# Optimization experiments

Measured on AMD Instinct MI355X. Metric: run time of the kernel, lower is better.

Reference implementation:

```python
import jax, jax.numpy as jnp
import numpy as np

N_NODES = 100000
N_EDGES = 1600000
D_IN = 13      # per-localization feature dim
D_POS = 3
HIDDEN = 64
D_OUT = 64


def setup_inputs() -> dict:
    key = jax.random.key(0)
    ks = jax.random.split(key, 6)
    x_locs = jax.random.normal(ks[0], (N_NODES, D_IN), dtype=jnp.float32)
    pos_locs = jax.random.uniform(ks[1], (N_NODES, D_POS), dtype=jnp.float32)
    edge_index = jax.random.randint(ks[2], (2, N_EDGES), 0, N_NODES, dtype=jnp.int64)
    fan1 = D_IN + D_POS
    W1 = jax.random.normal(ks[3], (fan1, HIDDEN), dtype=jnp.float32) / np.sqrt(fan1)
    b1 = jnp.zeros((HIDDEN,), dtype=jnp.float32)
    W2 = jax.random.normal(ks[4], (HIDDEN, D_OUT), dtype=jnp.float32) / np.sqrt(HIDDEN)
    b2 = jnp.zeros((D_OUT,), dtype=jnp.float32)
    return {"x_locs": x_locs, "pos_locs": pos_locs, "W1": W1, "b1": b1,
            "W2": W2, "b2": b2, "edge_index": edge_index}


def reference(x_locs, pos_locs, W1, b1, W2, b2, edge_index):
    # PointNetConv (source_to_target): j = edge_index[0] (source), i = edge_index[1] (target)
    src = edge_index[0]
    dst = edge_index[1]
    # message input: [x_j, pos_j - pos_i]  -> [E, D_IN + D_POS]
    msg_in = jnp.concatenate([x_locs[src], pos_locs[src] - pos_locs[dst]], axis=-1)
    # local_nn: Linear -> ReLU -> Linear
    h = jax.nn.relu(msg_in @ W1 + b1)            # [E, HIDDEN]
    h = h @ W2 + b2                               # [E, D_OUT]
    # max aggregation per target node; empty segments get -inf
    agg = jax.ops.segment_max(h, dst, num_segments=N_NODES)  # [N, D_OUT]
    # final .relu() in LocEncoder; also maps empty (-inf) segments to 0 (PyG convention)
    return jax.nn.relu(agg)
```

## Files before the change

### kernel.cpp

```cpp
#include <hip/hip_runtime.h>


#define N_NODES 100000
#define N_EDGES 1600000
#define NB2  1563
#define NBLK 391
#define BATCH 4096
#define SCAP2 1280

typedef _Float16 half8 __attribute__((ext_vector_type(8)));
typedef float float4v __attribute__((ext_vector_type(4)));

__device__ inline int wave_incl_scan(int v, int lane) {
#pragma unroll
    for (int d = 1; d < 64; d <<= 1) {
        const int t = __shfl_up(v, d);
        if (lane >= d) v += t;
    }
    return v;
}

__global__ __launch_bounds__(256) void precompute_kernel(
    const float* __restrict__ x, const float* __restrict__ pos,
    const float* __restrict__ W1, const float* __restrict__ b1,
    _Float16* __restrict__ u16, _Float16* __restrict__ w16)
{
    const int lane = threadIdx.x & 63;
    float w1c[16];
#pragma unroll
    for (int k = 0; k < 16; ++k) w1c[k] = W1[k * 64 + lane];
    const float b1c = b1[lane];

    const int waveId = blockIdx.x * 4 + (threadIdx.x >> 6);
    const int step   = 512 * 4 * 2;

    for (int nd = waveId * 2; nd < N_NODES; nd += step) {
        const int nA = nd, nB = nd + 1;
        float mA = 0.f, mB = 0.f;
        if (lane < 13) {
            mA = x[nA * 13 + lane];
            mB = x[nB * 13 + lane];
        } else if (lane < 16) {
            mA = pos[nA * 3 + (lane - 13)];
            mB = pos[nB * 3 + (lane - 13)];
        }

        float aA = b1c, wA = 0.f, aB = b1c, wB = 0.f;
#pragma unroll
        for (int k = 0; k < 13; ++k) {
            aA = fmaf(__shfl(mA, k), w1c[k], aA);
            aB = fmaf(__shfl(mB, k), w1c[k], aB);
        }
#pragma unroll
        for (int k = 13; k < 16; ++k) {
            const float pA = __shfl(mA, k), pB = __shfl(mB, k);
            aA = fmaf(pA, w1c[k], aA);  wA = fmaf(pA, w1c[k], wA);
            aB = fmaf(pB, w1c[k], aB);  wB = fmaf(pB, w1c[k], wB);
        }
        u16[nA * 64 + lane] = (_Float16)aA;
        w16[nA * 64 + lane] = (_Float16)wA;
        u16[nB * 64 + lane] = (_Float16)aB;
        w16[nB * 64 + lane] = (_Float16)wB;
    }
}

__global__ __launch_bounds__(256) void partition_kernel(
    const int* __restrict__ ei,
    int* __restrict__ offsT,
    int* __restrict__ blockSorted)
{
    __shared__ int hist[NB2], eoff[NB2], offc[NB2];
    __shared__ int csumP[25];

    const int tid  = threadIdx.x;
    const int lane = tid & 63;
    const int wv   = tid >> 6;
    const int blk  = blockIdx.x;
    const int e0   = blk * BATCH;
    const int nn   = (N_EDGES - e0) < BATCH ? (N_EDGES - e0) : BATCH;

    for (int i = tid; i < NB2; i += 256) hist[i] = 0;
    __syncthreads();

#pragma unroll
    for (int rep = 0; rep < 4; ++rep) {
        const int base = rep * 1024 + tid * 4;
        if (base < nn) {
            const int4 d4 = *(const int4*)(ei + N_EDGES + e0 + base);
            atomicAdd(&hist[d4.x >> 6], 1);
            atomicAdd(&hist[d4.y >> 6], 1);
            atomicAdd(&hist[d4.z >> 6], 1);
            atomicAdd(&hist[d4.w >> 6], 1);
        }
    }
    __syncthreads();

    for (int c = wv; c < 25; c += 4) {
        const int idx = c * 64 + lane;
        const int val = (idx < NB2) ? hist[idx] : 0;
        const int inc = wave_incl_scan(val, lane);
        if (idx < NB2) eoff[idx] = inc;
        if (lane == 63) csumP[c] = inc;
    }
    __syncthreads();
    if (tid == 0) {
        int a = 0;
#pragma unroll
        for (int c = 0; c < 25; ++c) { const int t = csumP[c]; csumP[c] = a; a += t; }
    }
    __syncthreads();
    for (int c = wv; c < 25; c += 4) {
        const int idx = c * 64 + lane;
        if (idx < NB2) eoff[idx] += csumP[c] - hist[idx];
    }
    __syncthreads();

    for (int b = tid; b < NB2; b += 256) {
        offsT[b * NBLK + blk] = eoff[b];
        offc[b] = eoff[b];
    }
    if (tid == 0) offsT[NB2 * NBLK + blk] = nn;
    __syncthreads();

    int* dstp = blockSorted + blk * BATCH;
#pragma unroll
    for (int rep = 0; rep < 4; ++rep) {
        const int base = rep * 1024 + tid * 4;
        if (base < nn) {
            const int4 s4 = *(const int4*)(ei + e0 + base);
            const int4 d4 = *(const int4*)(ei + N_EDGES + e0 + base);
            int p;
            p = atomicAdd(&offc[d4.x >> 6], 1); dstp[p] = (s4.x << 6) | (d4.x & 63);
            p = atomicAdd(&offc[d4.y >> 6], 1); dstp[p] = (s4.y << 6) | (d4.y & 63);
            p = atomicAdd(&offc[d4.z >> 6], 1); dstp[p] = (s4.z << 6) | (d4.z & 63);
            p = atomicAdd(&offc[d4.w >> 6], 1); dstp[p] = (s4.w << 6) | (d4.w & 63);
        }
    }
}

__global__ __launch_bounds__(256, 4) void aggregate_kernel(
    const _Float16* __restrict__ u16,
    const _Float16* __restrict__ w16,
    const float* __restrict__ W2,
    const float* __restrict__ b2,
    const int*   __restrict__ offsT,
    const int*   __restrict__ blockSorted,
    float*       __restrict__ out)
{
    __shared__ int staged[SCAP2];
    __shared__ int sortedL[SCAP2];
    __shared__ int E[NBLK], G[NBLK];
    __shared__ int hist[64], nstart[64], hoff[64];
    __shared__ int csum[8];
    __shared__ int totT;

    const int tid  = threadIdx.x;
    const int lane = tid & 63;
    const int wv   = tid >> 6;
    const int q = lane >> 4, n = lane & 15;
    const int b = blockIdx.x;
    const int node0 = b * 64;

    half8 w2f[2][4];
#pragma unroll
    for (int s = 0; s < 2; ++s)
#pragma unroll
        for (int t = 0; t < 4; ++t)
#pragma unroll
            for (int j = 0; j < 8; ++j)
                w2f[s][t][j] = (_Float16)W2[(s * 32 + q * 8 + j) * 64 + (n + 16 * t)];
    float b2c[4];
#pragma unroll
    for (int t = 0; t < 4; ++t) b2c[t] = b2[n + 16 * t];

    if (tid < 64) hist[tid] = 0;

    for (int r = tid; r < NBLK; r += 256) {
        const int lo = offsT[b * NBLK + r];
        const int hi = offsT[(b + 1) * NBLK + r];
        staged[r] = hi - lo;
        G[r] = r * BATCH + lo;
    }
    __syncthreads();
    for (int c = wv; c < 7; c += 4) {
        const int idx = c * 64 + lane;
        const int val = (idx < NBLK) ? staged[idx] : 0;
        const int inc = wave_incl_scan(val, lane);
        if (idx < NBLK) E[idx] = inc;
        if (lane == 63) csum[c] = inc;
    }
    __syncthreads();
    if (tid == 0) {
        int a = 0;
#pragma unroll
        for (int c = 0; c < 7; ++c) { const int t = csum[c]; csum[c] = a; a += t; }
        totT = a;
    }
    __syncthreads();
    for (int c = wv; c < 7; c += 4) {
        const int idx = c * 64 + lane;
        if (idx < NBLK) E[idx] += csum[c] - staged[idx];
    }
    __syncthreads();

    int T = totT; T = T < SCAP2 ? T : SCAP2;

    for (int i = tid; i < T; i += 256) {
        int lo = 0, hi = NBLK - 1;
#pragma unroll
        for (int s = 0; s < 9; ++s) {
            const int mid = (lo + hi + 1) >> 1;
            if (E[mid] <= i) lo = mid; else hi = mid - 1;
        }
        const int w = blockSorted[G[lo] + (i - E[lo])];
        staged[i] = w;
        atomicAdd(&hist[w & 63], 1);
    }
    __syncthreads();

    if (wv == 0) {
        const int v = hist[lane];
        const int inc = wave_incl_scan(v, lane);
        nstart[lane] = inc - v;
        hoff[lane]   = inc - v;
    }
    __syncthreads();
    for (int i = tid; i < T; i += 256) {
        const int w = staged[i];
        const int p = atomicAdd(&hoff[w & 63], 1);
        sortedL[p] = w >> 6;
    }
    __syncthreads();

    const half8 zero8 = {0, 0, 0, 0, 0, 0, 0, 0};

    auto compute = [&](int node, int2 sd, int src,
                       half8 ulo, half8 uhi, half8 wl, half8 wh) {
        float vmax[4] = {0.f, 0.f, 0.f, 0.f};
        int base = 0;
        while (true) {
            const int rows = (sd.y - base) < 16 ? (sd.y - base) : 16;
            if (rows > 0) {
                const half8 alo = __builtin_elementwise_max(ulo - wl, zero8);
                const half8 ahi = __builtin_elementwise_max(uhi - wh, zero8);
                float4v c2[4];
#pragma unroll
                for (int t = 0; t < 4; ++t) {
                    c2[t] = __builtin_amdgcn_mfma_f32_16x16x32_f16(
                        alo, w2f[0][t], (float4v){0.f, 0.f, 0.f, 0.f}, 0, 0, 0);
                    c2[t] = __builtin_amdgcn_mfma_f32_16x16x32_f16(
                        ahi, w2f[1][t], c2[t], 0, 0, 0);
                }
#pragma unroll
                for (int r = 0; r < 4; ++r) {
                    const int row = q * 4 + r;
#pragma unroll
                    for (int t = 0; t < 4; ++t) {
                        const float v = c2[t][r] + b2c[t];
                        if (row < rows) vmax[t] = fmaxf(vmax[t], v);
                    }
                }
            }
            base += 16;
            if (base >= sd.y) break;
            const int r2 = (sd.y - base) < 16 ? (sd.y - base) : 16;
            src = (n < r2) ? sortedL[sd.x + base + n] : 0;
            ulo = *(const half8*)(u16 + src * 64 + q * 8);
            uhi = *(const half8*)(u16 + src * 64 + 32 + q * 8);
        }
#pragma unroll
        for (int t = 0; t < 4; ++t) {
            vmax[t] = fmaxf(vmax[t], __shfl_xor(vmax[t], 16));
            vmax[t] = fmaxf(vmax[t], __shfl_xor(vmax[t], 32));
        }
        float v = vmax[0];
        v = (q == 1) ? vmax[1] : v;
        v = (q == 2) ? vmax[2] : v;
        v = (q == 3) ? vmax[3] : v;
        if (node < N_NODES) out[node * 64 + lane] = v;
    };

    const int nlbase = wv * 16;
#pragma unroll 1
    for (int g = 0; g < 16; g += 2) {
        const int nlA = nlbase + g, nlB = nlA + 1;
        const int nA = node0 + nlA, nB = node0 + nlB;
        const int2 sdA = {nstart[nlA], hist[nlA]};
        const int2 sdB = {nstart[nlB], hist[nlB]};
        const int nAc = nA < (N_NODES - 1) ? nA : (N_NODES - 1);
        const int nBc = nB < (N_NODES - 1) ? nB : (N_NODES - 1);

        const int rA = sdA.y < 16 ? sdA.y : 16;
        const int rB = sdB.y < 16 ? sdB.y : 16;
        const int srcA = (n < rA) ? sortedL[sdA.x + n] : 0;
        const int srcB = (n < rB) ? sortedL[sdB.x + n] : 0;

        const half8 ulA = *(const half8*)(u16 + srcA * 64 + q * 8);
        const half8 uhA = *(const half8*)(u16 + srcA * 64 + 32 + q * 8);
        const half8 wlA = *(const half8*)(w16 + nAc * 64 + q * 8);
        const half8 whA = *(const half8*)(w16 + nAc * 64 + 32 + q * 8);
        const half8 ulB = *(const half8*)(u16 + srcB * 64 + q * 8);
        const half8 uhB = *(const half8*)(u16 + srcB * 64 + 32 + q * 8);
        const half8 wlB = *(const half8*)(w16 + nBc * 64 + q * 8);
        const half8 whB = *(const half8*)(w16 + nBc * 64 + 32 + q * 8);

        compute(nA, sdA, srcA, ulA, uhA, wlA, whA);
        compute(nB, sdB, srcB, ulB, uhB, wlB, whB);
    }
}

extern "C" void kernel_launch(void* const* d_in, const int* in_sizes, int n_in,
                              void* d_out, int out_size, void* d_ws, size_t ws_size,
                              hipStream_t stream) {
    const float* x   = (const float*)d_in[0];
    const float* pos = (const float*)d_in[1];
    const float* W1  = (const float*)d_in[2];
    const float* b1  = (const float*)d_in[3];
    const float* W2  = (const float*)d_in[4];
    const float* b2  = (const float*)d_in[5];
    const int*   ei  = (const int*)d_in[6];

    char* ws = (char*)d_ws;
    int* blockSorted = (int*)(ws + 0);
    int* offsT       = (int*)(ws + 6406144);
    _Float16* u16 = (_Float16*)(ws + 8852480);
    _Float16* w16 = (_Float16*)(ws + 21652480);

    precompute_kernel<<<512, 256, 0, stream>>>(x, pos, W1, b1, u16, w16);
    partition_kernel<<<NBLK, 256, 0, stream>>>(ei, offsT, blockSorted);
    aggregate_kernel<<<NB2, 256, 0, stream>>>(
        u16, w16, W2, b2, offsT, blockSorted, (float*)d_out);
}
```

Measured before the change: 193.1 us.

## Replace two-level partition with global atomic bucket scatter into fixed-capacity bins

Replaces the per-batch local sort, which wrote transposed offset tables, with a single scatter kernel. It uses global atomics on per-bucket counters to write edges straight into fixed-capacity (1280) bins per 64-node group. The aggregate kernel then reads its bin contiguously, with no prefix scans or binary search. This cuts the partition work and the indirect gathers. The cost is heavy contention on global atomics across 1563 counters, an extra memset launch, and silently dropped edges if a bin overflows its capacity (the old code also capped at 1280).

```diff
diff --git a/kernel.cpp b/kernel.cpp
--- a/kernel.cpp
+++ b/kernel.cpp
@@ -4,9 +4,7 @@
 #define N_NODES 100000
 #define N_EDGES 1600000
 #define NB2  1563
-#define NBLK 391
-#define BATCH 4096
-#define SCAP2 1280
+#define CAP  1280
 
 typedef _Float16 half8 __attribute__((ext_vector_type(8)));
 typedef float float4v __attribute__((ext_vector_type(4)));
@@ -64,78 +62,24 @@
     }
 }
 
-__global__ __launch_bounds__(256) void partition_kernel(
+__global__ __launch_bounds__(256) void scatter_kernel(
     const int* __restrict__ ei,
-    int* __restrict__ offsT,
-    int* __restrict__ blockSorted)
+    int* __restrict__ gcnt,
+    int* __restrict__ sortedG)
 {
-    __shared__ int hist[NB2], eoff[NB2], offc[NB2];
-    __shared__ int csumP[25];
-
-    const int tid  = threadIdx.x;
-    const int lane = tid & 63;
-    const int wv   = tid >> 6;
-    const int blk  = blockIdx.x;
-    const int e0   = blk * BATCH;
-    const int nn   = (N_EDGES - e0) < BATCH ? (N_EDGES - e0) : BATCH;
-
-    for (int i = tid; i < NB2; i += 256) hist[i] = 0;
-    __syncthreads();
-
-#pragma unroll
-    for (int rep = 0; rep < 4; ++rep) {
-        const int base = rep * 1024 + tid * 4;
-        if (base < nn) {
-            const int4 d4 = *(const int4*)(ei + N_EDGES + e0 + base);
-            atomicAdd(&hist[d4.x >> 6], 1);
-            atomicAdd(&hist[d4.y >> 6], 1);
-            atomicAdd(&hist[d4.z >> 6], 1);
-            atomicAdd(&hist[d4.w >> 6], 1);
-        }
-    }
-    __syncthreads();
-
-    for (int c = wv; c < 25; c += 4) {
-        const int idx = c * 64 + lane;
-        const int val = (idx < NB2) ? hist[idx] : 0;
-        const int inc = wave_incl_scan(val, lane);
-        if (idx < NB2) eoff[idx] = inc;
-        if (lane == 63) csumP[c] = inc;
-    }
-    __syncthreads();
-    if (tid == 0) {
-        int a = 0;
-#pragma unroll
-        for (int c = 0; c < 25; ++c) { const int t = csumP[c]; csumP[c] = a; a += t; }
-    }
-    __syncthreads();
-    for (int c = wv; c < 25; c += 4) {
-        const int idx = c * 64 + lane;
-        if (idx < NB2) eoff[idx] += csumP[c] - hist[idx];
-    }
-    __syncthreads();
-
-    for (int b = tid; b < NB2; b += 256) {
-        offsT[b * NBLK + blk] = eoff[b];
-        offc[b] = eoff[b];
-    }
-    if (tid == 0) offsT[NB2 * NBLK + blk] = nn;
-    __syncthreads();
-
-    int* dstp = blockSorted + blk * BATCH;
-#pragma unroll
-    for (int rep = 0; rep < 4; ++rep) {
-        const int base = rep * 1024 + tid * 4;
-        if (base < nn) {
-            const int4 s4 = *(const int4*)(ei + e0 + base);
-            const int4 d4 = *(const int4*)(ei + N_EDGES + e0 + base);
-            int p;
-            p = atomicAdd(&offc[d4.x >> 6], 1); dstp[p] = (s4.x << 6) | (d4.x & 63);
-            p = atomicAdd(&offc[d4.y >> 6], 1); dstp[p] = (s4.y << 6) | (d4.y & 63);
-            p = atomicAdd(&offc[d4.z >> 6], 1); dstp[p] = (s4.z << 6) | (d4.z & 63);
-            p = atomicAdd(&offc[d4.w >> 6], 1); dstp[p] = (s4.w << 6) | (d4.w & 63);
-        }
-    }
+    const int base = (blockIdx.x * 256 + threadIdx.x) * 4;
+    if (base >= N_EDGES) return;
+    const int4 s4 = *(const int4*)(ei + base);
+    const int4 d4 = *(const int4*)(ei + N_EDGES + base);
+    int b, p;
+    b = d4.x >> 6; p = atomicAdd(&gcnt[b], 1);
+    if (p < CAP) sortedG[b * CAP + p] = (s4.x << 6) | (d4.x & 63);
+    b = d4.y >> 6; p = atomicAdd(&gcnt[b], 1);
+    if (p < CAP) sortedG[b * CAP + p] = (s4.y << 6) | (d4.y & 63);
+    b = d4.z >> 6; p = atomicAdd(&gcnt[b], 1);
+    if (p < CAP) sortedG[b * CAP + p] = (s4.z << 6) | (d4.z & 63);
+    b = d4.w >> 6; p = atomicAdd(&gcnt[b], 1);
+    if (p < CAP) sortedG[b * CAP + p] = (s4.w << 6) | (d4.w & 63);
 }
 
 __global__ __launch_bounds__(256, 4) void aggregate_kernel(
@@ -143,16 +87,13 @@
     const _Float16* __restrict__ w16,
     const float* __restrict__ W2,
     const float* __restrict__ b2,
-    const int*   __restrict__ offsT,
-    const int*   __restrict__ blockSorted,
+    const int*   __restrict__ gcnt,
+    const int*   __restrict__ sortedG,
     float*       __restrict__ out)
 {
-    __shared__ int staged[SCAP2];
-    __shared__ int sortedL[SCAP2];
-    __shared__ int E[NBLK], G[NBLK];
+    __shared__ int staged[CAP];
+    __shared__ int sortedL[CAP];
     __shared__ int hist[64], nstart[64], hoff[64];
-    __shared__ int csum[8];
-    __shared__ int totT;
 
     const int tid  = threadIdx.x;
     const int lane = tid & 63;
@@ -174,47 +115,19 @@
     for (int t = 0; t < 4; ++t) b2c[t] = b2[n + 16 * t];
 
     if (tid < 64) hist[tid] = 0;
-
-    for (int r = tid; r < NBLK; r += 256) {
-        const int lo = offsT[b * NBLK + r];
-        const int hi = offsT[(b + 1) * NBLK + r];
-        staged[r] = hi - lo;
-        G[r] = r * BATCH + lo;
-    }
-    __syncthreads();
-    for (int c = wv; c < 7; c += 4) {
-        const int idx = c * 64 + lane;
-        const int val = (idx < NBLK) ? staged[idx] : 0;
-        const int inc = wave_incl_scan(val, lane);
-        if (idx < NBLK) E[idx] = inc;
-        if (lane == 63) csum[c] = inc;
-    }
-    __syncthreads();
-    if (tid == 0) {
-        int a = 0;
-#pragma unroll
-        for (int c = 0; c < 7; ++c) { const int t = csum[c]; csum[c] = a; a += t; }
-        totT = a;
-    }
-    __syncthreads();
-    for (int c = wv; c < 7; c += 4) {
-        const int idx = c * 64 + lane;
-        if (idx < NBLK) E[idx] += csum[c] - staged[idx];
-    }
-    __syncthreads();
-
-    int T = totT; T = T < SCAP2 ? T : SCAP2;
-
-    for (int i = tid; i < T; i += 256) {
-        int lo = 0, hi = NBLK - 1;
-#pragma unroll
-        for (int s = 0; s < 9; ++s) {
-            const int mid = (lo + hi + 1) >> 1;
-            if (E[mid] <= i) lo = mid; else hi = mid - 1;
-        }
-        const int w = blockSorted[G[lo] + (i - E[lo])];
-        staged[i] = w;
-        atomicAdd(&hist[w & 63], 1);
+    __syncthreads();
+
+    const int cnt = gcnt[b];
+    const int T = cnt < CAP ? cnt : CAP;
+
+    const int nI4 = (T + 3) >> 2;
+    for (int i4 = tid; i4 < nI4; i4 += 256) {
+        const int4 v = *(const int4*)(sortedG + b * CAP + i4 * 4);
+        const int e0 = i4 * 4;
+        if (e0 + 0 < T) { staged[e0 + 0] = v.x; atomicAdd(&hist[v.x & 63], 1); }
+        if (e0 + 1 < T) { staged[e0 + 1] = v.y; atomicAdd(&hist[v.y & 63], 1); }
+        if (e0 + 2 < T) { staged[e0 + 2] = v.z; atomicAdd(&hist[v.z & 63], 1); }
+        if (e0 + 3 < T) { staged[e0 + 3] = v.w; atomicAdd(&hist[v.w & 63], 1); }
     }
     __syncthreads();
 
@@ -321,13 +234,14 @@
     const int*   ei  = (const int*)d_in[6];
 
     char* ws = (char*)d_ws;
-    int* blockSorted = (int*)(ws + 0);
-    int* offsT       = (int*)(ws + 6406144);
-    _Float16* u16 = (_Float16*)(ws + 8852480);
-    _Float16* w16 = (_Float16*)(ws + 21652480);
-
+    int* gcnt    = (int*)(ws + 0);
+    int* sortedG = (int*)(ws + 8192);
+    _Float16* u16 = (_Float16*)(ws + 8010752);
+    _Float16* w16 = (_Float16*)(ws + 20810752);
+
+    hipMemsetAsync(gcnt, 0, NB2 * sizeof(int), stream);
     precompute_kernel<<<512, 256, 0, stream>>>(x, pos, W1, b1, u16, w16);
-    partition_kernel<<<NBLK, 256, 0, stream>>>(ei, offsT, blockSorted);
+    scatter_kernel<<<1563, 256, 0, stream>>>(ei, gcnt, sortedG);
     aggregate_kernel<<<NB2, 256, 0, stream>>>(
-        u16, w16, W2, b2, offsT, blockSorted, (float*)d_out);
-}
+        u16, w16, W2, b2, gcnt, sortedG, (float*)d_out);
+}
```

New measurement: 409.8 us. +112.3%, slower.
